# Kernel optimization log

Measured on AMD Instinct MI355X. Metric: run time of the kernel, lower is better.

Reference implementation:

```python
import jax, jax.numpy as jnp
import numpy as np

B, N, D, H, O = 256, 1024, 512, 2048, 512


def setup_inputs() -> dict:
    key = jax.random.key(0)
    ks = jax.random.split(key, 6)
    x = jax.random.normal(ks[0], (B, N, D), dtype=jnp.float32)
    # binary float mask [B,N,1]; ensure every set has >=1 unpadded element
    mask = (jax.random.uniform(ks[1], (B, N, 1)) < 0.9).astype(jnp.float32)
    mask = mask.at[:, :1, :].set(1.0)
    # per-row (4B rows after stat-concat) unpadded counts in [1, N]
    unpadded = jax.random.randint(ks[2], (4 * B, 1), 1, N + 1).astype(jnp.float32)
    W1 = jax.random.normal(ks[3], (D, H), dtype=jnp.float32) * (1.0 / np.sqrt(D))
    b1 = jnp.zeros((H,), jnp.float32)
    W2 = jax.random.normal(ks[4], (H, O), dtype=jnp.float32) * (1.0 / np.sqrt(H))
    b2 = jnp.zeros((O,), jnp.float32)
    return dict(x=x, mask=mask, unpadded=unpadded, W1=W1, b1=b1, W2=W2, b2=b2)


def reference(x, mask, unpadded, W1, b1, W2, b2):
    # x: [B,N,D], mask: [B,N,1] (0/1 float)
    neg_inf = jnp.float32(-jnp.inf)
    cnt = mask.sum(axis=1)                              # [B,1]
    mean = (x * mask).sum(axis=1) / cnt                 # [B,D]
    agg_max = jnp.where(mask > 0, x, neg_inf).max(axis=1)   # [B,D]
    agg_min = -jnp.where(mask > 0, -x, neg_inf).max(axis=1) # [B,D]
    var = (jnp.square(x - mean[:, None, :]) * mask).sum(axis=1) / cnt
    std = jnp.sqrt(var)                                 # [B,D]
    aggr = jnp.concatenate([mean, agg_max, agg_min, std], axis=0)  # [4B,D]
    # faithful to source: delta = sum(unpadded)/unpadded.shape[1] + 1 (scalar)
    delta = unpadded.sum() / unpadded.shape[1] + 1.0
    logu = jnp.log(unpadded + 1.0)                      # [4B,1]
    amplification = aggr * (logu / delta)
    attenuation = aggr * (delta / logu)
    scale_concat = jnp.concatenate([aggr, amplification, attenuation], axis=0)  # [12B,D]
    h = jax.nn.relu(scale_concat @ W1 + b1)
    return h @ W2 + b2                                  # [12B,O]
```

## Files before the change

### kernel.cpp

```cpp
#include <hip/hip_runtime.h>
#include <hip/hip_bf16.h>
#include <math.h>
#include <stdint.h>

#define B_  256
#define N_  1024
#define D_  512
#define H_  2048
#define O_  512
#define M4  (4 * B_)
#define M12 (12 * B_)
#define NCH 8

typedef __attribute__((ext_vector_type(8))) short short8;
typedef __attribute__((ext_vector_type(4))) float f32x4;
typedef unsigned short ushort_t;

__device__ inline uint32_t pkbf(float a, float b) {
    union { __hip_bfloat162 h; uint32_t u; } cv;
    cv.h = __float22bfloat162_rn(float2{a, b});
    return cv.u;
}

__device__ inline void load_lds16(const void* g, void* l) {
    typedef const __attribute__((address_space(1))) uint32_t* gp_t;
    typedef __attribute__((address_space(3))) uint32_t* lp_t;
    __builtin_amdgcn_global_load_lds((gp_t)(uintptr_t)g, (lp_t)(uint32_t)(uintptr_t)l,
                                     16, 0, 0);
}

__device__ __forceinline__ void agg_core(const float* __restrict__ x,
                                         const float* __restrict__ mask,
                                         float* __restrict__ part,
                                         float* __restrict__ cntp,
                                         int id, int t) {
    const int b    = id >> 2;
    const int c    = id & 3;
    const int half = t >> 7;
    const int d4   = (t & 127) << 2;
    const float* base = x + ((size_t)b * N_ + (size_t)c * 256) * D_ + d4;
    const float* mp   = mask + (size_t)b * N_ + (size_t)c * 256;

    f32x4 sum = {0.f,0.f,0.f,0.f}, sq = {0.f,0.f,0.f,0.f};
    f32x4 mx = {-INFINITY,-INFINITY,-INFINITY,-INFINITY};
    f32x4 mn = { INFINITY, INFINITY, INFINITY, INFINITY};
    float cnt = 0.f;

    #pragma unroll 8
    for (int n = half; n < 256; n += 2) {
        float m = mp[n];
        f32x4 v = __builtin_nontemporal_load((const f32x4*)(base + (size_t)n * D_));
        sum.x = fmaf(v.x, m, sum.x); sum.y = fmaf(v.y, m, sum.y);
        sum.z = fmaf(v.z, m, sum.z); sum.w = fmaf(v.w, m, sum.w);
        sq.x  = fmaf(v.x * v.x, m, sq.x); sq.y = fmaf(v.y * v.y, m, sq.y);
        sq.z  = fmaf(v.z * v.z, m, sq.z); sq.w = fmaf(v.w * v.w, m, sq.w);
        cnt  += m;
        bool um = m > 0.f;
        mx.x = um ? fmaxf(mx.x, v.x) : mx.x; mx.y = um ? fmaxf(mx.y, v.y) : mx.y;
        mx.z = um ? fmaxf(mx.z, v.z) : mx.z; mx.w = um ? fmaxf(mx.w, v.w) : mx.w;
        mn.x = um ? fminf(mn.x, v.x) : mn.x; mn.y = um ? fminf(mn.y, v.y) : mn.y;
        mn.z = um ? fminf(mn.z, v.z) : mn.z; mn.w = um ? fminf(mn.w, v.w) : mn.w;
    }

    const int ch = c * 2 + half;
    const size_t SS = (size_t)B_ * NCH * D_;
    const size_t pi = ((size_t)(b * NCH + ch)) * D_ + d4;
    *(f32x4*)(part + 0 * SS + pi) = sum;
    *(f32x4*)(part + 1 * SS + pi) = sq;
    *(f32x4*)(part + 2 * SS + pi) = mx;
    *(f32x4*)(part + 3 * SS + pi) = mn;
    if ((t & 127) == 0) cntp[b * NCH + ch] = cnt;
}

__device__ void conv_tile(const float* __restrict__ in, ushort_t* __restrict__ out,
                          int R, int C, int bx, int by, float* tile ) {
    const int t  = threadIdx.x;
    const int r0 = by << 5;
    const int c0 = bx << 5;
    const int tr = t >> 3;
    const int tc = (t & 7) << 2;

    float4 v = *(const float4*)(in + (size_t)(r0 + tr) * C + c0 + tc);
    tile[tr * 33 + tc + 0] = v.x; tile[tr * 33 + tc + 1] = v.y;
    tile[tr * 33 + tc + 2] = v.z; tile[tr * 33 + tc + 3] = v.w;
    __syncthreads();

    union { uint32_t u[2]; ushort4 us; } o;
    o.u[0] = pkbf(tile[(tc + 0) * 33 + tr], tile[(tc + 1) * 33 + tr]);
    o.u[1] = pkbf(tile[(tc + 2) * 33 + tr], tile[(tc + 3) * 33 + tr]);
    *(ushort4*)(out + (size_t)(c0 + tr) * R + r0 + tc) = o.us;
}

__global__ __launch_bounds__(256) void k1_mega(const float* __restrict__ x,
                                               const float* __restrict__ mask,
                                               const float* __restrict__ W1,
                                               const float* __restrict__ W2,
                                               const float* __restrict__ unpadded,
                                               float* __restrict__ part,
                                               float* __restrict__ cntp,
                                               ushort_t* __restrict__ W1t,
                                               ushort_t* __restrict__ W2t,
                                               float* __restrict__ scale) {
    __shared__ float smem[32 * 33];
    const int id = blockIdx.x;
    const int t  = threadIdx.x;

    if (id < 1024) {
        agg_core(x, mask, part, cntp, id, t);
    } else if (id < 2048) {
        const int tid = id - 1024;
        conv_tile(W1, W1t, D_, H_, tid & 63, tid >> 6, smem);
    } else if (id < 3072) {
        const int tid = id - 2048;
        conv_tile(W2, W2t, H_, O_, tid & 15, tid >> 4, smem);
    } else {
        float4 u4 = *(const float4*)(unpadded + t * 4);
        smem[t] = u4.x + u4.y + u4.z + u4.w;
        __syncthreads();
        for (int s = 128; s > 0; s >>= 1) {
            if (t < s) smem[t] += smem[t + s];
            __syncthreads();
        }
        const float delta = smem[0] + 1.0f;
        float uu[4] = {u4.x, u4.y, u4.z, u4.w};
        #pragma unroll
        for (int j = 0; j < 4; ++j) {
            const int i = t * 4 + j;
            const float logu = logf(uu[j] + 1.0f);
            scale[i]          = 1.0f;
            scale[M4 + i]     = logu / delta;
            scale[2 * M4 + i] = delta / logu;
        }
    }
}

__global__ __launch_bounds__(256) void agg_final(const float* __restrict__ part,
                                                 const float* __restrict__ cntp,
                                                 ushort_t* __restrict__ aggr) {
    const int b = blockIdx.x;
    const int t = threadIdx.x;
    const int d = 2 * t;

    float cnt = 0.f;
    #pragma unroll
    for (int c = 0; c < NCH; ++c) cnt += cntp[b * NCH + c];

    const size_t SS = (size_t)B_ * NCH * D_;
    float2 sum = {0.f, 0.f}, sq = {0.f, 0.f};
    float2 mx = {-INFINITY, -INFINITY}, mn = {INFINITY, INFINITY};
    #pragma unroll
    for (int c = 0; c < NCH; ++c) {
        const size_t pi = ((size_t)(b * NCH + c)) * D_ + d;
        float2 s  = *(const float2*)(part + 0 * SS + pi);
        float2 q  = *(const float2*)(part + 1 * SS + pi);
        float2 vx = *(const float2*)(part + 2 * SS + pi);
        float2 vn = *(const float2*)(part + 3 * SS + pi);
        sum.x += s.x; sum.y += s.y;
        sq.x  += q.x; sq.y  += q.y;
        mx.x = fmaxf(mx.x, vx.x); mx.y = fmaxf(mx.y, vx.y);
        mn.x = fminf(mn.x, vn.x); mn.y = fminf(mn.y, vn.y);
    }
    const float ic = 1.f / cnt;
    float2 mean = {sum.x * ic, sum.y * ic};
    float2 var  = {fmaxf(sq.x * ic - mean.x * mean.x, 0.f),
                   fmaxf(sq.y * ic - mean.y * mean.y, 0.f)};

    *(uint32_t*)(aggr + (size_t)(0 * B_ + b) * D_ + d) = pkbf(mean.x, mean.y);
    *(uint32_t*)(aggr + (size_t)(1 * B_ + b) * D_ + d) = pkbf(mx.x, mx.y);
    *(uint32_t*)(aggr + (size_t)(2 * B_ + b) * D_ + d) = pkbf(mn.x, mn.y);
    *(uint32_t*)(aggr + (size_t)(3 * B_ + b) * D_ + d) = pkbf(sqrtf(var.x), sqrtf(var.y));
}

__global__ __launch_bounds__(256) void gemm1(const ushort_t* __restrict__ A,
                                             const ushort_t* __restrict__ Bt,
                                             float* __restrict__ C) {
    __shared__ ushort_t As0[64 * 64], As1[64 * 64];
    __shared__ ushort_t Bs0[64 * 64], Bs1[64 * 64];

    const int t    = threadIdx.x;
    const int wave = t >> 6;
    const int lane = t & 63;
    const int wm   = wave >> 1, wn = wave & 1;
    const int row0 = blockIdx.y << 6;
    const int col0 = blockIdx.x << 6;

    const int lr  = lane >> 3;
    const int ksw = ((lane & 7) ^ lr) << 3;

    const int rl = lane & 15;
    const int hi = lane >> 4;

    const ushort_t* Ag0 = A  + (size_t)(row0 + wave * 8 + lr) * D_ + ksw;
    const ushort_t* Ag1 = A  + (size_t)(row0 + 32 + wave * 8 + lr) * D_ + ksw;
    const ushort_t* Bg0 = Bt + (size_t)(col0 + wave * 8 + lr) * D_ + ksw;
    const ushort_t* Bg1 = Bt + (size_t)(col0 + 32 + wave * 8 + lr) * D_ + ksw;
    const int ld0 = (wave * 8) * 64;
    const int ld1 = (32 + wave * 8) * 64;

    f32x4 acc[2][2] = {};

    ushort_t* Ac = As0; ushort_t* An = As1;
    ushort_t* Bc = Bs0; ushort_t* Bn = Bs1;

    load_lds16(Ag0, Ac + ld0); load_lds16(Ag1, Ac + ld1);
    load_lds16(Bg0, Bc + ld0); load_lds16(Bg1, Bc + ld1);
    __syncthreads();

    for (int tt = 0; tt < D_ / 64; ++tt) {
        const int k1 = (tt + 1) * 64;
        if (tt + 1 < D_ / 64) {
            load_lds16(Ag0 + k1, An + ld0); load_lds16(Ag1 + k1, An + ld1);
            load_lds16(Bg0 + k1, Bn + ld0); load_lds16(Bg1 + k1, Bn + ld1);
        }
        short8 av[2][2], bv[2][2];
        #pragma unroll
        for (int i = 0; i < 2; ++i) {
            const int ra = wm * 32 + i * 16 + rl;
            const int rb = wn * 32 + i * 16 + rl;
            #pragma unroll
            for (int k2 = 0; k2 < 2; ++k2) {
                av[i][k2] = *(const short8*)(Ac + ra * 64 + (((k2 * 4 + hi) ^ (ra & 7)) << 3));
                bv[i][k2] = *(const short8*)(Bc + rb * 64 + (((k2 * 4 + hi) ^ (rb & 7)) << 3));
            }
        }
        #pragma unroll
        for (int i = 0; i < 2; ++i)
            #pragma unroll
            for (int j = 0; j < 2; ++j)
                #pragma unroll
                for (int k2 = 0; k2 < 2; ++k2)
                    acc[i][j] = __builtin_amdgcn_mfma_f32_16x16x32_bf16(av[i][k2], bv[j][k2], acc[i][j], 0, 0, 0);
        __syncthreads();
        ushort_t* tp;
        tp = Ac; Ac = An; An = tp;
        tp = Bc; Bc = Bn; Bn = tp;
    }

    #pragma unroll
    for (int i = 0; i < 2; ++i)
        #pragma unroll
        for (int j = 0; j < 2; ++j) {
            const int col = col0 + wn * 32 + j * 16 + rl;
            #pragma unroll
            for (int v = 0; v < 4; ++v) {
                const int row = row0 + wm * 32 + i * 16 + hi * 4 + v;
                C[(size_t)row * H_ + col] = acc[i][j][v];
            }
        }
}

__global__ __launch_bounds__(256) void gemm2_fused(const float* __restrict__ Z,
                                                   const float* __restrict__ scale,
                                                   const float* __restrict__ b1,
                                                   const ushort_t* __restrict__ W2t,
                                                   const float* __restrict__ b2,
                                                   float* __restrict__ out) {
    __shared__ ushort_t As0[64 * 64],  As1[64 * 64];
    __shared__ ushort_t Bs0[64 * 64],  Bs1[64 * 64];

    const int t    = threadIdx.x;
    const int wave = t >> 6;
    const int lane = t & 63;
    const int wm   = wave >> 1, wn = wave & 1;

    const int id  = blockIdx.x;
    const int xcd = id & 7;
    const int idx = id >> 3;
    const int rb  = xcd * 6 + (idx % 6);
    const int cb  = idx / 6;
    const int row0 = rb << 6;
    const int col0 = cb << 6;

    const int arow = t >> 2;
    const int asi  = t & 3;
    const float s  = scale[row0 + arow];
    const float* Zrow = Z + (size_t)((row0 + arow) & (M4 - 1)) * H_ + asi * 8;
    const float* b1p  = b1 + asi * 8;
    const int aw0 = arow * 64 + ((asi ^ (arow & 7)) << 3);
    const int aw1 = arow * 64 + (((asi + 4) ^ (arow & 7)) << 3);

    const int lr  = lane >> 3;
    const int ksw = ((lane & 7) ^ lr) << 3;
    const ushort_t* Bg0 = W2t + (size_t)(col0 + wave * 8 + lr) * H_ + ksw;
    const ushort_t* Bg1 = W2t + (size_t)(col0 + 32 + wave * 8 + lr) * H_ + ksw;
    const int ld0 = (wave * 8) * 64;
    const int ld1 = (32 + wave * 8) * 64;

    const int rl = lane & 15;
    const int hi = lane >> 4;

    f32x4 acc[2][2] = {};

    ushort_t* Ac = As0; ushort_t* An = As1;
    ushort_t* Bc = Bs0; ushort_t* Bn = Bs1;

    {
        load_lds16(Bg0, Bc + ld0); load_lds16(Bg1, Bc + ld1);
        float4 z0 = *(const float4*)(Zrow);
        float4 z1 = *(const float4*)(Zrow + 4);
        float4 z2 = *(const float4*)(Zrow + 32);
        float4 z3 = *(const float4*)(Zrow + 36);
        float4 c0 = *(const float4*)(b1p);
        float4 c1 = *(const float4*)(b1p + 4);
        float4 c2 = *(const float4*)(b1p + 32);
        float4 c3 = *(const float4*)(b1p + 36);
        union { uint32_t u[4]; short8 s8; } h0, h1;
        h0.u[0] = pkbf(fmaxf(fmaf(s, z0.x, c0.x), 0.f), fmaxf(fmaf(s, z0.y, c0.y), 0.f));
        h0.u[1] = pkbf(fmaxf(fmaf(s, z0.z, c0.z), 0.f), fmaxf(fmaf(s, z0.w, c0.w), 0.f));
        h0.u[2] = pkbf(fmaxf(fmaf(s, z1.x, c1.x), 0.f), fmaxf(fmaf(s, z1.y, c1.y), 0.f));
        h0.u[3] = pkbf(fmaxf(fmaf(s, z1.z, c1.z), 0.f), fmaxf(fmaf(s, z1.w, c1.w), 0.f));
        h1.u[0] = pkbf(fmaxf(fmaf(s, z2.x, c2.x), 0.f), fmaxf(fmaf(s, z2.y, c2.y), 0.f));
        h1.u[1] = pkbf(fmaxf(fmaf(s, z2.z, c2.z), 0.f), fmaxf(fmaf(s, z2.w, c2.w), 0.f));
        h1.u[2] = pkbf(fmaxf(fmaf(s, z3.x, c3.x), 0.f), fmaxf(fmaf(s, z3.y, c3.y), 0.f));
        h1.u[3] = pkbf(fmaxf(fmaf(s, z3.z, c3.z), 0.f), fmaxf(fmaf(s, z3.w, c3.w), 0.f));
        *(short8*)(Ac + aw0) = h0.s8;
        *(short8*)(Ac + aw1) = h1.s8;
        __syncthreads();
    }

    for (int tt = 0; tt < H_ / 64; ++tt) {
        const int k1 = (tt + 1) * 64;
        const bool more = (tt + 1 < H_ / 64);
        float4 z0, z1, z2, z3, c0, c1, c2, c3;
        if (more) {
            load_lds16(Bg0 + k1, Bn + ld0); load_lds16(Bg1 + k1, Bn + ld1);
            z0 = *(const float4*)(Zrow + k1);
            z1 = *(const float4*)(Zrow + k1 + 4);
            z2 = *(const float4*)(Zrow + k1 + 32);
            z3 = *(const float4*)(Zrow + k1 + 36);
            c0 = *(const float4*)(b1p + k1);
            c1 = *(const float4*)(b1p + k1 + 4);
            c2 = *(const float4*)(b1p + k1 + 32);
            c3 = *(const float4*)(b1p + k1 + 36);
        }

        short8 av[2][2], bv[2][2];
        #pragma unroll
        for (int i = 0; i < 2; ++i) {
            const int ra = wm * 32 + i * 16 + rl;
            const int rb2 = wn * 32 + i * 16 + rl;
            #pragma unroll
            for (int k2 = 0; k2 < 2; ++k2) {
                av[i][k2] = *(const short8*)(Ac + ra * 64 + (((k2 * 4 + hi) ^ (ra & 7)) << 3));
                bv[i][k2] = *(const short8*)(Bc + rb2 * 64 + (((k2 * 4 + hi) ^ (rb2 & 7)) << 3));
            }
        }
        #pragma unroll
        for (int i = 0; i < 2; ++i)
            #pragma unroll
            for (int j = 0; j < 2; ++j)
                #pragma unroll
                for (int k2 = 0; k2 < 2; ++k2)
                    acc[i][j] = __builtin_amdgcn_mfma_f32_16x16x32_bf16(av[i][k2], bv[j][k2], acc[i][j], 0, 0, 0);

        if (more) {
            union { uint32_t u[4]; short8 s8; } h0, h1;
            h0.u[0] = pkbf(fmaxf(fmaf(s, z0.x, c0.x), 0.f), fmaxf(fmaf(s, z0.y, c0.y), 0.f));
            h0.u[1] = pkbf(fmaxf(fmaf(s, z0.z, c0.z), 0.f), fmaxf(fmaf(s, z0.w, c0.w), 0.f));
            h0.u[2] = pkbf(fmaxf(fmaf(s, z1.x, c1.x), 0.f), fmaxf(fmaf(s, z1.y, c1.y), 0.f));
            h0.u[3] = pkbf(fmaxf(fmaf(s, z1.z, c1.z), 0.f), fmaxf(fmaf(s, z1.w, c1.w), 0.f));
            h1.u[0] = pkbf(fmaxf(fmaf(s, z2.x, c2.x), 0.f), fmaxf(fmaf(s, z2.y, c2.y), 0.f));
            h1.u[1] = pkbf(fmaxf(fmaf(s, z2.z, c2.z), 0.f), fmaxf(fmaf(s, z2.w, c2.w), 0.f));
            h1.u[2] = pkbf(fmaxf(fmaf(s, z3.x, c3.x), 0.f), fmaxf(fmaf(s, z3.y, c3.y), 0.f));
            h1.u[3] = pkbf(fmaxf(fmaf(s, z3.z, c3.z), 0.f), fmaxf(fmaf(s, z3.w, c3.w), 0.f));
            *(short8*)(An + aw0) = h0.s8;
            *(short8*)(An + aw1) = h1.s8;
        }
        __syncthreads();
        ushort_t* tp;
        tp = Ac; Ac = An; An = tp;
        tp = Bc; Bc = Bn; Bn = tp;
    }

    #pragma unroll
    for (int i = 0; i < 2; ++i)
        #pragma unroll
        for (int j = 0; j < 2; ++j) {
            const int col = col0 + wn * 32 + j * 16 + rl;
            const float bb = b2[col];
            #pragma unroll
            for (int v = 0; v < 4; ++v) {
                const int row = row0 + wm * 32 + i * 16 + hi * 4 + v;
                out[(size_t)row * O_ + col] = acc[i][j][v] + bb;
            }
        }
}

extern "C" void kernel_launch(void* const* d_in, const int* in_sizes, int n_in,
                              void* d_out, int out_size, void* d_ws, size_t ws_size,
                              hipStream_t stream) {
    const float* x        = (const float*)d_in[0];
    const float* mask     = (const float*)d_in[1];
    const float* unpadded = (const float*)d_in[2];
    const float* W1       = (const float*)d_in[3];
    const float* b1       = (const float*)d_in[4];
    const float* W2       = (const float*)d_in[5];
    const float* b2       = (const float*)d_in[6];
    float* out = (float*)d_out;

    float* ws = (float*)d_ws;
    float* part  = ws;
    float* cntp  = ws + 4194304;
    float* scale = ws + 4196352;
    float* Z     = ws + 4199424;
    ushort_t* bfw  = (ushort_t*)(ws + 6296576);
    ushort_t* W1t  = bfw;
    ushort_t* W2t  = bfw + 1048576;
    ushort_t* aggr = bfw + 2097152;

    k1_mega<<<3073, 256, 0, stream>>>(x, mask, W1, W2, unpadded,
                                      part, cntp, W1t, W2t, scale);
    agg_final<<<B_, 256, 0, stream>>>(part, cntp, aggr);
    gemm1<<<dim3(H_ / 64, M4 / 64), 256, 0, stream>>>(aggr, W1t, Z);
    gemm2_fused<<<384, 256, 0, stream>>>(Z, scale, b1, W2t, b2, out);
}
```

Measured before the change: 139.5 us.

## Move scale/bias/ReLU epilogue into gemm1 and split-K gemm2 across wave groups

gemm1 now applies the three per-row scales, bias and ReLU in its epilogue and writes the full 12B x H hidden matrix as bf16. gemm2 therefore becomes a plain bf16 GEMM that loads A directly into LDS. gemm2 also uses 512 threads with two wave groups, each covering half of K, and the partial sums are combined through LDS. This removes the per-tile fp32 Z reads and conversion work inside gemm2's main loop and doubles waves per block. The cost is a larger bf16 write from gemm1, made of scattered 2-byte stores, plus an extra LDS reduction and barrier.

```diff
diff --git a/kernel.cpp b/kernel.cpp
--- a/kernel.cpp
+++ b/kernel.cpp
@@ -20,6 +20,11 @@
     union { __hip_bfloat162 h; uint32_t u; } cv;
     cv.h = __float22bfloat162_rn(float2{a, b});
     return cv.u;
+}
+__device__ inline ushort_t f2bf(float f) {
+    union { float f; uint32_t u; } v; v.f = f;
+    uint32_t r = v.u + 0x7FFFu + ((v.u >> 16) & 1u);
+    return (ushort_t)(r >> 16);
 }
 
 __device__ inline void load_lds16(const void* g, void* l) {
@@ -171,9 +176,11 @@
     *(uint32_t*)(aggr + (size_t)(3 * B_ + b) * D_ + d) = pkbf(sqrtf(var.x), sqrtf(var.y));
 }
 
-__global__ __launch_bounds__(256) void gemm1(const ushort_t* __restrict__ A,
-                                             const ushort_t* __restrict__ Bt,
-                                             float* __restrict__ C) {
+__global__ __launch_bounds__(256) void gemm1_h(const ushort_t* __restrict__ A,
+                                               const ushort_t* __restrict__ Bt,
+                                               const float* __restrict__ scale,
+                                               const float* __restrict__ b1,
+                                               ushort_t* __restrict__ h) {
     __shared__ ushort_t As0[64 * 64], As1[64 * 64];
     __shared__ ushort_t Bs0[64 * 64], Bs1[64 * 64];
 
@@ -237,31 +244,38 @@
     }
 
     #pragma unroll
-    for (int i = 0; i < 2; ++i)
-        #pragma unroll
-        for (int j = 0; j < 2; ++j) {
-            const int col = col0 + wn * 32 + j * 16 + rl;
-            #pragma unroll
-            for (int v = 0; v < 4; ++v) {
-                const int row = row0 + wm * 32 + i * 16 + hi * 4 + v;
-                C[(size_t)row * H_ + col] = acc[i][j][v];
+    for (int i = 0; i < 2; ++i) {
+        #pragma unroll
+        for (int v = 0; v < 4; ++v) {
+            const int row = row0 + wm * 32 + i * 16 + hi * 4 + v;
+            const float s1 = scale[M4 + row];
+            const float s2 = scale[2 * M4 + row];
+            #pragma unroll
+            for (int j = 0; j < 2; ++j) {
+                const int col = col0 + wn * 32 + j * 16 + rl;
+                const float bb = b1[col];
+                const float z  = acc[i][j][v];
+                h[(size_t)row * H_ + col]            = f2bf(fmaxf(z + bb, 0.f));
+                h[(size_t)(M4 + row) * H_ + col]     = f2bf(fmaxf(fmaf(s1, z, bb), 0.f));
+                h[(size_t)(2 * M4 + row) * H_ + col] = f2bf(fmaxf(fmaf(s2, z, bb), 0.f));
             }
         }
-}
-
-__global__ __launch_bounds__(256) void gemm2_fused(const float* __restrict__ Z,
-                                                   const float* __restrict__ scale,
-                                                   const float* __restrict__ b1,
-                                                   const ushort_t* __restrict__ W2t,
-                                                   const float* __restrict__ b2,
-                                                   float* __restrict__ out) {
-    __shared__ ushort_t As0[64 * 64],  As1[64 * 64];
-    __shared__ ushort_t Bs0[64 * 64],  Bs1[64 * 64];
+    }
+}
+
+__global__ __launch_bounds__(512) void gemm2_pure(const ushort_t* __restrict__ h,
+                                                  const ushort_t* __restrict__ W2t,
+                                                  const float* __restrict__ b2,
+                                                  float* __restrict__ out) {
+    __shared__ ushort_t As[2][2][64 * 64];
+    __shared__ ushort_t Bs[2][2][64 * 64];
 
     const int t    = threadIdx.x;
     const int wave = t >> 6;
+    const int kg   = wave >> 2;
+    const int w4   = wave & 3;
     const int lane = t & 63;
-    const int wm   = wave >> 1, wn = wave & 1;
+    const int wm   = w4 >> 1, wn = w4 & 1;
 
     const int id  = blockIdx.x;
     const int xcd = id & 7;
@@ -271,69 +285,35 @@
     const int row0 = rb << 6;
     const int col0 = cb << 6;
 
-    const int arow = t >> 2;
-    const int asi  = t & 3;
-    const float s  = scale[row0 + arow];
-    const float* Zrow = Z + (size_t)((row0 + arow) & (M4 - 1)) * H_ + asi * 8;
-    const float* b1p  = b1 + asi * 8;
-    const int aw0 = arow * 64 + ((asi ^ (arow & 7)) << 3);
-    const int aw1 = arow * 64 + (((asi + 4) ^ (arow & 7)) << 3);
-
     const int lr  = lane >> 3;
     const int ksw = ((lane & 7) ^ lr) << 3;
-    const ushort_t* Bg0 = W2t + (size_t)(col0 + wave * 8 + lr) * H_ + ksw;
-    const ushort_t* Bg1 = W2t + (size_t)(col0 + 32 + wave * 8 + lr) * H_ + ksw;
-    const int ld0 = (wave * 8) * 64;
-    const int ld1 = (32 + wave * 8) * 64;
+    const int kbase = kg * (H_ / 2);
+
+    const ushort_t* Ag0 = h   + (size_t)(row0 + w4 * 8 + lr) * H_ + kbase + ksw;
+    const ushort_t* Ag1 = h   + (size_t)(row0 + 32 + w4 * 8 + lr) * H_ + kbase + ksw;
+    const ushort_t* Bg0 = W2t + (size_t)(col0 + w4 * 8 + lr) * H_ + kbase + ksw;
+    const ushort_t* Bg1 = W2t + (size_t)(col0 + 32 + w4 * 8 + lr) * H_ + kbase + ksw;
+    const int ld0 = (w4 * 8) * 64;
+    const int ld1 = (32 + w4 * 8) * 64;
 
     const int rl = lane & 15;
     const int hi = lane >> 4;
 
     f32x4 acc[2][2] = {};
 
-    ushort_t* Ac = As0; ushort_t* An = As1;
-    ushort_t* Bc = Bs0; ushort_t* Bn = Bs1;
-
-    {
-        load_lds16(Bg0, Bc + ld0); load_lds16(Bg1, Bc + ld1);
-        float4 z0 = *(const float4*)(Zrow);
-        float4 z1 = *(const float4*)(Zrow + 4);
-        float4 z2 = *(const float4*)(Zrow + 32);
-        float4 z3 = *(const float4*)(Zrow + 36);
-        float4 c0 = *(const float4*)(b1p);
-        float4 c1 = *(const float4*)(b1p + 4);
-        float4 c2 = *(const float4*)(b1p + 32);
-        float4 c3 = *(const float4*)(b1p + 36);
-        union { uint32_t u[4]; short8 s8; } h0, h1;
-        h0.u[0] = pkbf(fmaxf(fmaf(s, z0.x, c0.x), 0.f), fmaxf(fmaf(s, z0.y, c0.y), 0.f));
-        h0.u[1] = pkbf(fmaxf(fmaf(s, z0.z, c0.z), 0.f), fmaxf(fmaf(s, z0.w, c0.w), 0.f));
-        h0.u[2] = pkbf(fmaxf(fmaf(s, z1.x, c1.x), 0.f), fmaxf(fmaf(s, z1.y, c1.y), 0.f));
-        h0.u[3] = pkbf(fmaxf(fmaf(s, z1.z, c1.z), 0.f), fmaxf(fmaf(s, z1.w, c1.w), 0.f));
-        h1.u[0] = pkbf(fmaxf(fmaf(s, z2.x, c2.x), 0.f), fmaxf(fmaf(s, z2.y, c2.y), 0.f));
-        h1.u[1] = pkbf(fmaxf(fmaf(s, z2.z, c2.z), 0.f), fmaxf(fmaf(s, z2.w, c2.w), 0.f));
-        h1.u[2] = pkbf(fmaxf(fmaf(s, z3.x, c3.x), 0.f), fmaxf(fmaf(s, z3.y, c3.y), 0.f));
-        h1.u[3] = pkbf(fmaxf(fmaf(s, z3.z, c3.z), 0.f), fmaxf(fmaf(s, z3.w, c3.w), 0.f));
-        *(short8*)(Ac + aw0) = h0.s8;
-        *(short8*)(Ac + aw1) = h1.s8;
-        __syncthreads();
-    }
-
-    for (int tt = 0; tt < H_ / 64; ++tt) {
+    ushort_t* Ac = &As[kg][0][0]; ushort_t* An = &As[kg][1][0];
+    ushort_t* Bc = &Bs[kg][0][0]; ushort_t* Bn = &Bs[kg][1][0];
+
+    load_lds16(Ag0, Ac + ld0); load_lds16(Ag1, Ac + ld1);
+    load_lds16(Bg0, Bc + ld0); load_lds16(Bg1, Bc + ld1);
+    __syncthreads();
+
+    for (int tt = 0; tt < 16; ++tt) {
         const int k1 = (tt + 1) * 64;
-        const bool more = (tt + 1 < H_ / 64);
-        float4 z0, z1, z2, z3, c0, c1, c2, c3;
-        if (more) {
+        if (tt + 1 < 16) {
+            load_lds16(Ag0 + k1, An + ld0); load_lds16(Ag1 + k1, An + ld1);
             load_lds16(Bg0 + k1, Bn + ld0); load_lds16(Bg1 + k1, Bn + ld1);
-            z0 = *(const float4*)(Zrow + k1);
-            z1 = *(const float4*)(Zrow + k1 + 4);
-            z2 = *(const float4*)(Zrow + k1 + 32);
-            z3 = *(const float4*)(Zrow + k1 + 36);
-            c0 = *(const float4*)(b1p + k1);
-            c1 = *(const float4*)(b1p + k1 + 4);
-            c2 = *(const float4*)(b1p + k1 + 32);
-            c3 = *(const float4*)(b1p + k1 + 36);
-        }
-
+        }
         short8 av[2][2], bv[2][2];
         #pragma unroll
         for (int i = 0; i < 2; ++i) {
@@ -352,38 +332,39 @@
                 #pragma unroll
                 for (int k2 = 0; k2 < 2; ++k2)
                     acc[i][j] = __builtin_amdgcn_mfma_f32_16x16x32_bf16(av[i][k2], bv[j][k2], acc[i][j], 0, 0, 0);
-
-        if (more) {
-            union { uint32_t u[4]; short8 s8; } h0, h1;
-            h0.u[0] = pkbf(fmaxf(fmaf(s, z0.x, c0.x), 0.f), fmaxf(fmaf(s, z0.y, c0.y), 0.f));
-            h0.u[1] = pkbf(fmaxf(fmaf(s, z0.z, c0.z), 0.f), fmaxf(fmaf(s, z0.w, c0.w), 0.f));
-            h0.u[2] = pkbf(fmaxf(fmaf(s, z1.x, c1.x), 0.f), fmaxf(fmaf(s, z1.y, c1.y), 0.f));
-            h0.u[3] = pkbf(fmaxf(fmaf(s, z1.z, c1.z), 0.f), fmaxf(fmaf(s, z1.w, c1.w), 0.f));
-            h1.u[0] = pkbf(fmaxf(fmaf(s, z2.x, c2.x), 0.f), fmaxf(fmaf(s, z2.y, c2.y), 0.f));
-            h1.u[1] = pkbf(fmaxf(fmaf(s, z2.z, c2.z), 0.f), fmaxf(fmaf(s, z2.w, c2.w), 0.f));
-            h1.u[2] = pkbf(fmaxf(fmaf(s, z3.x, c3.x), 0.f), fmaxf(fmaf(s, z3.y, c3.y), 0.f));
-            h1.u[3] = pkbf(fmaxf(fmaf(s, z3.z, c3.z), 0.f), fmaxf(fmaf(s, z3.w, c3.w), 0.f));
-            *(short8*)(An + aw0) = h0.s8;
-            *(short8*)(An + aw1) = h1.s8;
-        }
         __syncthreads();
         ushort_t* tp;
         tp = Ac; Ac = An; An = tp;
         tp = Bc; Bc = Bn; Bn = tp;
     }
 
-    #pragma unroll
-    for (int i = 0; i < 2; ++i)
-        #pragma unroll
-        for (int j = 0; j < 2; ++j) {
-            const int col = col0 + wn * 32 + j * 16 + rl;
-            const float bb = b2[col];
-            #pragma unroll
-            for (int v = 0; v < 4; ++v) {
-                const int row = row0 + wm * 32 + i * 16 + hi * 4 + v;
-                out[(size_t)row * O_ + col] = acc[i][j][v] + bb;
+    float* red = (float*)&As[0][0][0];
+    const int fidx = w4 * 1024 + lane * 16;
+    if (kg == 1) {
+        #pragma unroll
+        for (int i = 0; i < 2; ++i)
+            #pragma unroll
+            for (int j = 0; j < 2; ++j)
+                #pragma unroll
+                for (int v = 0; v < 4; ++v)
+                    red[fidx + i * 8 + j * 4 + v] = acc[i][j][v];
+    }
+    __syncthreads();
+    if (kg == 0) {
+        #pragma unroll
+        for (int i = 0; i < 2; ++i)
+            #pragma unroll
+            for (int j = 0; j < 2; ++j) {
+                const int col = col0 + wn * 32 + j * 16 + rl;
+                const float bb = b2[col];
+                #pragma unroll
+                for (int v = 0; v < 4; ++v) {
+                    const int row = row0 + wm * 32 + i * 16 + hi * 4 + v;
+                    out[(size_t)row * O_ + col] =
+                        acc[i][j][v] + red[fidx + i * 8 + j * 4 + v] + bb;
+                }
             }
-        }
+    }
 }
 
 extern "C" void kernel_launch(void* const* d_in, const int* in_sizes, int n_in,
@@ -402,15 +383,15 @@
     float* part  = ws;
     float* cntp  = ws + 4194304;
     float* scale = ws + 4196352;
-    float* Z     = ws + 4199424;
-    ushort_t* bfw  = (ushort_t*)(ws + 6296576);
+    ushort_t* bfw  = (ushort_t*)(ws + 4200448);
     ushort_t* W1t  = bfw;
     ushort_t* W2t  = bfw + 1048576;
     ushort_t* aggr = bfw + 2097152;
+    ushort_t* h    = bfw + 2621440;
 
     k1_mega<<<3073, 256, 0, stream>>>(x, mask, W1, W2, unpadded,
                                       part, cntp, W1t, W2t, scale);
     agg_final<<<B_, 256, 0, stream>>>(part, cntp, aggr);
-    gemm1<<<dim3(H_ / 64, M4 / 64), 256, 0, stream>>>(aggr, W1t, Z);
-    gemm2_fused<<<384, 256, 0, stream>>>(Z, scale, b1, W2t, b2, out);
-}
+    gemm1_h<<<dim3(H_ / 64, M4 / 64), 256, 0, stream>>>(aggr, W1t, scale, b1, h);
+    gemm2_pure<<<384, 512, 0, stream>>>(h, W2t, b2, out);
+}
```

Measured after the change: 126.3 us. 9.4% less time.
